# Optimization experiments

Measured on AMD Instinct MI355X. Metric: run time of the kernel, lower is better.

## Reference

```python
import jax, jax.numpy as jnp
import numpy as np

THRESHOLD = 0.01


def setup_inputs() -> dict:
    key = jax.random.key(0)
    kv_cache = jax.random.normal(key, (2, 16, 8192, 128), dtype=jnp.float32)
    return {"kv_cache": kv_cache}


def _dequantize_bin(kv, binmask, levels):
    # min/max restricted to the bin via +-inf sentinels (no dynamic shapes)
    inf = jnp.float32(jnp.inf)
    bmin = jnp.min(jnp.where(binmask, kv, inf))
    bmax = jnp.max(jnp.where(binmask, kv, -inf))
    has_any = jnp.any(binmask)
    valid = has_any & (bmax != bmin)
    denom = jnp.where(valid, bmax - bmin, jnp.float32(1.0))  # safe denom
    q = jnp.round((kv - bmin) / denom * levels)
    deq = q / levels * denom + bmin
    return jnp.where(binmask & valid, deq, kv)


def reference(kv_cache):
    mask = jnp.abs(kv_cache) > THRESHOLD  # large-value bin
    out = _dequantize_bin(kv_cache, ~mask, jnp.float32(15.0))   # small bin: 4-bit
    out = jnp.where(mask, _dequantize_bin(kv_cache, mask, jnp.float32(255.0)), out)  # large bin: 8-bit
    return out
```

## Files before the change

kernel.cpp:

```cpp
#include <hip/hip_runtime.h>

static constexpr float kThresh = 0.01f;
static constexpr int RBLOCKS = 1024;

__device__ __forceinline__ unsigned fkey(float f) {
    unsigned u = __float_as_uint(f);
    return (u & 0x80000000u) ? ~u : (u | 0x80000000u);
}
__device__ __forceinline__ float unkey(unsigned k) {
    unsigned u = (k & 0x80000000u) ? (k & 0x7fffffffu) : ~k;
    return __uint_as_float(u);
}

__device__ __forceinline__ void acc_one(float x, unsigned& smin, unsigned& smax,
                                        unsigned& lmin, unsigned& lmax) {
    unsigned k = fkey(x);
    if (fabsf(x) > kThresh) {
        lmin = min(lmin, k);
        lmax = max(lmax, k);
    } else {
        smin = min(smin, k);
        smax = max(smax, k);
    }
}

__device__ __forceinline__ void wave_reduce4(unsigned& smin, unsigned& smax,
                                             unsigned& lmin, unsigned& lmax) {
    #pragma unroll
    for (int off = 32; off > 0; off >>= 1) {
        smin = min(smin, (unsigned)__shfl_down((int)smin, off));
        smax = max(smax, (unsigned)__shfl_down((int)smax, off));
        lmin = min(lmin, (unsigned)__shfl_down((int)lmin, off));
        lmax = max(lmax, (unsigned)__shfl_down((int)lmax, off));
    }
}

__global__ __launch_bounds__(256) void kv_partial(const float* __restrict__ in, int n,
                                                  unsigned* __restrict__ partials) {
    unsigned smin = 0xFFFFFFFFu, smax = 0u, lmin = 0xFFFFFFFFu, lmax = 0u;
    const int n4 = n >> 2;
    const float4* __restrict__ in4 = (const float4*)in;
    const int stride = gridDim.x * blockDim.x;
    for (int i = blockIdx.x * blockDim.x + threadIdx.x; i < n4; i += stride) {
        float4 v = in4[i];
        acc_one(v.x, smin, smax, lmin, lmax);
        acc_one(v.y, smin, smax, lmin, lmax);
        acc_one(v.z, smin, smax, lmin, lmax);
        acc_one(v.w, smin, smax, lmin, lmax);
    }
    for (int i = (n4 << 2) + blockIdx.x * blockDim.x + threadIdx.x; i < n; i += stride) {
        acc_one(in[i], smin, smax, lmin, lmax);
    }

    wave_reduce4(smin, smax, lmin, lmax);

    __shared__ unsigned ls[4][4];
    const int wave = threadIdx.x >> 6;
    if ((threadIdx.x & 63) == 0) {
        ls[wave][0] = smin; ls[wave][1] = smax; ls[wave][2] = lmin; ls[wave][3] = lmax;
    }
    __syncthreads();
    if (threadIdx.x == 0) {
        unsigned a = ls[0][0], b = ls[0][1], c = ls[0][2], d = ls[0][3];
        #pragma unroll
        for (int w = 1; w < 4; ++w) {
            a = min(a, ls[w][0]); b = max(b, ls[w][1]);
            c = min(c, ls[w][2]); d = max(d, ls[w][3]);
        }
        partials[blockIdx.x * 4 + 0] = a;
        partials[blockIdx.x * 4 + 1] = b;
        partials[blockIdx.x * 4 + 2] = c;
        partials[blockIdx.x * 4 + 3] = d;
    }
}

__global__ __launch_bounds__(256) void kv_final(const unsigned* __restrict__ partials,
                                                unsigned* __restrict__ ws) {
    unsigned smin = 0xFFFFFFFFu, smax = 0u, lmin = 0xFFFFFFFFu, lmax = 0u;
    for (int i = threadIdx.x; i < RBLOCKS; i += 256) {
        smin = min(smin, partials[4 * i + 0]);
        smax = max(smax, partials[4 * i + 1]);
        lmin = min(lmin, partials[4 * i + 2]);
        lmax = max(lmax, partials[4 * i + 3]);
    }
    wave_reduce4(smin, smax, lmin, lmax);

    __shared__ unsigned ls[4][4];
    const int wave = threadIdx.x >> 6;
    if ((threadIdx.x & 63) == 0) {
        ls[wave][0] = smin; ls[wave][1] = smax; ls[wave][2] = lmin; ls[wave][3] = lmax;
    }
    __syncthreads();
    if (threadIdx.x == 0) {
        unsigned a = ls[0][0], b = ls[0][1], c = ls[0][2], d = ls[0][3];
        #pragma unroll
        for (int w = 1; w < 4; ++w) {
            a = min(a, ls[w][0]); b = max(b, ls[w][1]);
            c = min(c, ls[w][2]); d = max(d, ls[w][3]);
        }
        ws[0] = a; ws[1] = b; ws[2] = c; ws[3] = d;
    }
}

__device__ __forceinline__ float deq1(float x, float smin, float ssc, float sis, bool sv,
                                      float lmin, float lsc, float lis, bool lv) {
    bool large = fabsf(x) > kThresh;
    float bmin = large ? lmin : smin;
    float sc   = large ? lsc : ssc;
    float is   = large ? lis : sis;
    bool  v    = large ? lv : sv;
    float q = rintf((x - bmin) * sc);
    float d = fmaf(q, is, bmin);
    return v ? d : x;
}

__global__ __launch_bounds__(256) void kv_dequant(const float* __restrict__ in,
                                                  float* __restrict__ out, int n,
                                                  const unsigned* __restrict__ ws) {
    const unsigned sk0 = ws[0], sk1 = ws[1], lk0 = ws[2], lk1 = ws[3];
    const bool sv = sk0 < sk1;
    const bool lv = lk0 < lk1;
    const float smin = unkey(sk0);
    const float sden = sv ? (unkey(sk1) - smin) : 1.0f;
    const float lmin = unkey(lk0);
    const float lden = lv ? (unkey(lk1) - lmin) : 1.0f;
    const float ssc = 15.0f / sden,  sis = sden / 15.0f;
    const float lsc = 255.0f / lden, lis = lden / 255.0f;

    const int n4 = n >> 2;
    const int i = blockIdx.x * blockDim.x + threadIdx.x;
    const float4* __restrict__ in4 = (const float4*)in;
    float4* __restrict__ out4 = (float4*)out;
    if (i < n4) {
        float4 v = in4[i];
        float4 r;
        r.x = deq1(v.x, smin, ssc, sis, sv, lmin, lsc, lis, lv);
        r.y = deq1(v.y, smin, ssc, sis, sv, lmin, lsc, lis, lv);
        r.z = deq1(v.z, smin, ssc, sis, sv, lmin, lsc, lis, lv);
        r.w = deq1(v.w, smin, ssc, sis, sv, lmin, lsc, lis, lv);
        out4[i] = r;
    }
    const int tail = n - (n4 << 2);
    if (i < tail) {
        int j = (n4 << 2) + i;
        out[j] = deq1(in[j], smin, ssc, sis, sv, lmin, lsc, lis, lv);
    }
}

extern "C" void kernel_launch(void* const* d_in, const int* in_sizes, int n_in,
                              void* d_out, int out_size, void* d_ws, size_t ws_size,
                              hipStream_t stream) {
    const float* in = (const float*)d_in[0];
    float* out = (float*)d_out;
    unsigned* ws = (unsigned*)d_ws;
    const int n = in_sizes[0];

    unsigned* partials = (unsigned*)d_out;

    kv_partial<<<RBLOCKS, 256, 0, stream>>>(in, n, partials);
    kv_final<<<1, 256, 0, stream>>>(partials, ws);

    const int n4 = n >> 2;
    int dblocks = (n4 + 255) / 256;
    if (dblocks < 1) dblocks = 1;
    kv_dequant<<<dblocks, 256, 0, stream>>>(in, out, n, ws);
}
```

Measured before the change: 243.9 us.

## Fuse min/max reduction and dequantize into one cooperative kernel with grid sync

Replaces the three-kernel sequence (partial reduce, final reduce, dequant) with one cooperative kernel. It computes per-block partials, does a grid-wide sync, has every block re-reduce the partials, then dequantizes with a grid-stride loop. The reduce loop is also unrolled by two to keep more loads in flight. This removes two launch gaps and the separate final pass, and the second read of the 64MB input may partly hit cache. It costs a grid barrier and a cooperative launch, and falls back to the old path if the launch fails or the workspace is too small.

```diff
diff --git a/kernel.cpp b/kernel.cpp
--- a/kernel.cpp
+++ b/kernel.cpp
@@ -1,6 +1,10 @@
 #include <hip/hip_runtime.h>
+#include <hip/hip_cooperative_groups.h>
+
+namespace cg = cooperative_groups;
 
 static constexpr float kThresh = 0.01f;
+static constexpr int FBLOCKS = 1024;
 static constexpr int RBLOCKS = 1024;
 
 __device__ __forceinline__ unsigned fkey(float f) {
@@ -24,6 +28,14 @@
     }
 }
 
+__device__ __forceinline__ void acc4(const float4& v, unsigned& smin, unsigned& smax,
+                                     unsigned& lmin, unsigned& lmax) {
+    acc_one(v.x, smin, smax, lmin, lmax);
+    acc_one(v.y, smin, smax, lmin, lmax);
+    acc_one(v.z, smin, smax, lmin, lmax);
+    acc_one(v.w, smin, smax, lmin, lmax);
+}
+
 __device__ __forceinline__ void wave_reduce4(unsigned& smin, unsigned& smax,
                                              unsigned& lmin, unsigned& lmax) {
     #pragma unroll
@@ -32,73 +44,6 @@
         smax = max(smax, (unsigned)__shfl_down((int)smax, off));
         lmin = min(lmin, (unsigned)__shfl_down((int)lmin, off));
         lmax = max(lmax, (unsigned)__shfl_down((int)lmax, off));
-    }
-}
-
-__global__ __launch_bounds__(256) void kv_partial(const float* __restrict__ in, int n,
-                                                  unsigned* __restrict__ partials) {
-    unsigned smin = 0xFFFFFFFFu, smax = 0u, lmin = 0xFFFFFFFFu, lmax = 0u;
-    const int n4 = n >> 2;
-    const float4* __restrict__ in4 = (const float4*)in;
-    const int stride = gridDim.x * blockDim.x;
-    for (int i = blockIdx.x * blockDim.x + threadIdx.x; i < n4; i += stride) {
-        float4 v = in4[i];
-        acc_one(v.x, smin, smax, lmin, lmax);
-        acc_one(v.y, smin, smax, lmin, lmax);
-        acc_one(v.z, smin, smax, lmin, lmax);
-        acc_one(v.w, smin, smax, lmin, lmax);
-    }
-    for (int i = (n4 << 2) + blockIdx.x * blockDim.x + threadIdx.x; i < n; i += stride) {
-        acc_one(in[i], smin, smax, lmin, lmax);
-    }
-
-    wave_reduce4(smin, smax, lmin, lmax);
-
-    __shared__ unsigned ls[4][4];
-    const int wave = threadIdx.x >> 6;
-    if ((threadIdx.x & 63) == 0) {
-        ls[wave][0] = smin; ls[wave][1] = smax; ls[wave][2] = lmin; ls[wave][3] = lmax;
-    }
-    __syncthreads();
-    if (threadIdx.x == 0) {
-        unsigned a = ls[0][0], b = ls[0][1], c = ls[0][2], d = ls[0][3];
-        #pragma unroll
-        for (int w = 1; w < 4; ++w) {
-            a = min(a, ls[w][0]); b = max(b, ls[w][1]);
-            c = min(c, ls[w][2]); d = max(d, ls[w][3]);
-        }
-        partials[blockIdx.x * 4 + 0] = a;
-        partials[blockIdx.x * 4 + 1] = b;
-        partials[blockIdx.x * 4 + 2] = c;
-        partials[blockIdx.x * 4 + 3] = d;
-    }
-}
-
-__global__ __launch_bounds__(256) void kv_final(const unsigned* __restrict__ partials,
-                                                unsigned* __restrict__ ws) {
-    unsigned smin = 0xFFFFFFFFu, smax = 0u, lmin = 0xFFFFFFFFu, lmax = 0u;
-    for (int i = threadIdx.x; i < RBLOCKS; i += 256) {
-        smin = min(smin, partials[4 * i + 0]);
-        smax = max(smax, partials[4 * i + 1]);
-        lmin = min(lmin, partials[4 * i + 2]);
-        lmax = max(lmax, partials[4 * i + 3]);
-    }
-    wave_reduce4(smin, smax, lmin, lmax);
-
-    __shared__ unsigned ls[4][4];
-    const int wave = threadIdx.x >> 6;
-    if ((threadIdx.x & 63) == 0) {
-        ls[wave][0] = smin; ls[wave][1] = smax; ls[wave][2] = lmin; ls[wave][3] = lmax;
-    }
-    __syncthreads();
-    if (threadIdx.x == 0) {
-        unsigned a = ls[0][0], b = ls[0][1], c = ls[0][2], d = ls[0][3];
-        #pragma unroll
-        for (int w = 1; w < 4; ++w) {
-            a = min(a, ls[w][0]); b = max(b, ls[w][1]);
-            c = min(c, ls[w][2]); d = max(d, ls[w][3]);
-        }
-        ws[0] = a; ws[1] = b; ws[2] = c; ws[3] = d;
     }
 }
 
@@ -112,6 +57,162 @@
     float q = rintf((x - bmin) * sc);
     float d = fmaf(q, is, bmin);
     return v ? d : x;
+}
+
+__global__ __launch_bounds__(256) void kv_fused(const float* __restrict__ in,
+                                                float* __restrict__ out, int n,
+                                                unsigned* __restrict__ ws) {
+    unsigned* __restrict__ partials = ws + 4;
+    const int n4 = n >> 2;
+    const float4* __restrict__ in4 = (const float4*)in;
+    const int stride = gridDim.x * blockDim.x;
+    const int i0 = blockIdx.x * blockDim.x + threadIdx.x;
+
+    unsigned smin = 0xFFFFFFFFu, smax = 0u, lmin = 0xFFFFFFFFu, lmax = 0u;
+    for (int i = i0; i < n4; i += 2 * stride) {
+        float4 a = in4[i];
+        int j = i + stride;
+        float4 b = (j < n4) ? in4[j] : a;
+        acc4(a, smin, smax, lmin, lmax);
+        acc4(b, smin, smax, lmin, lmax);
+    }
+    for (int i = (n4 << 2) + i0; i < n; i += stride) {
+        acc_one(in[i], smin, smax, lmin, lmax);
+    }
+
+    wave_reduce4(smin, smax, lmin, lmax);
+
+    __shared__ unsigned ls[4][4];
+    const int wave = threadIdx.x >> 6;
+    if ((threadIdx.x & 63) == 0) {
+        ls[wave][0] = smin; ls[wave][1] = smax; ls[wave][2] = lmin; ls[wave][3] = lmax;
+    }
+    __syncthreads();
+    if (threadIdx.x == 0) {
+        unsigned a = ls[0][0], b = ls[0][1], c = ls[0][2], d = ls[0][3];
+        #pragma unroll
+        for (int w = 1; w < 4; ++w) {
+            a = min(a, ls[w][0]); b = max(b, ls[w][1]);
+            c = min(c, ls[w][2]); d = max(d, ls[w][3]);
+        }
+        partials[blockIdx.x * 4 + 0] = a;
+        partials[blockIdx.x * 4 + 1] = b;
+        partials[blockIdx.x * 4 + 2] = c;
+        partials[blockIdx.x * 4 + 3] = d;
+    }
+
+    cg::this_grid().sync();
+
+    unsigned fa = 0xFFFFFFFFu, fb = 0u, fc = 0xFFFFFFFFu, fd = 0u;
+    for (int i = threadIdx.x; i < (int)gridDim.x; i += blockDim.x) {
+        fa = min(fa, partials[4 * i + 0]);
+        fb = max(fb, partials[4 * i + 1]);
+        fc = min(fc, partials[4 * i + 2]);
+        fd = max(fd, partials[4 * i + 3]);
+    }
+    wave_reduce4(fa, fb, fc, fd);
+    __syncthreads();
+    if ((threadIdx.x & 63) == 0) {
+        ls[wave][0] = fa; ls[wave][1] = fb; ls[wave][2] = fc; ls[wave][3] = fd;
+    }
+    __syncthreads();
+
+    __shared__ float p_smin, p_ssc, p_sis, p_lmin, p_lsc, p_lis;
+    __shared__ int p_sv, p_lv;
+    if (threadIdx.x == 0) {
+        unsigned a = ls[0][0], b = ls[0][1], c = ls[0][2], d = ls[0][3];
+        #pragma unroll
+        for (int w = 1; w < 4; ++w) {
+            a = min(a, ls[w][0]); b = max(b, ls[w][1]);
+            c = min(c, ls[w][2]); d = max(d, ls[w][3]);
+        }
+        bool sv = a < b, lv = c < d;
+        float smn = unkey(a), lmn = unkey(c);
+        float sden = sv ? (unkey(b) - smn) : 1.0f;
+        float lden = lv ? (unkey(d) - lmn) : 1.0f;
+        p_smin = smn; p_ssc = 15.0f / sden;  p_sis = sden / 15.0f;  p_sv = sv;
+        p_lmin = lmn; p_lsc = 255.0f / lden; p_lis = lden / 255.0f; p_lv = lv;
+    }
+    __syncthreads();
+
+    const float smn = p_smin, ssc = p_ssc, sis = p_sis;
+    const float lmn = p_lmin, lsc = p_lsc, lis = p_lis;
+    const bool sv = p_sv != 0, lv = p_lv != 0;
+
+    float4* __restrict__ out4 = (float4*)out;
+    for (int i = i0; i < n4; i += stride) {
+        float4 v = in4[i];
+        float4 r;
+        r.x = deq1(v.x, smn, ssc, sis, sv, lmn, lsc, lis, lv);
+        r.y = deq1(v.y, smn, ssc, sis, sv, lmn, lsc, lis, lv);
+        r.z = deq1(v.z, smn, ssc, sis, sv, lmn, lsc, lis, lv);
+        r.w = deq1(v.w, smn, ssc, sis, sv, lmn, lsc, lis, lv);
+        out4[i] = r;
+    }
+    for (int i = (n4 << 2) + i0; i < n; i += stride) {
+        out[i] = deq1(in[i], smn, ssc, sis, sv, lmn, lsc, lis, lv);
+    }
+}
+
+__global__ __launch_bounds__(256) void kv_partial(const float* __restrict__ in, int n,
+                                                  unsigned* __restrict__ partials) {
+    unsigned smin = 0xFFFFFFFFu, smax = 0u, lmin = 0xFFFFFFFFu, lmax = 0u;
+    const int n4 = n >> 2;
+    const float4* __restrict__ in4 = (const float4*)in;
+    const int stride = gridDim.x * blockDim.x;
+    for (int i = blockIdx.x * blockDim.x + threadIdx.x; i < n4; i += stride) {
+        float4 v = in4[i];
+        acc4(v, smin, smax, lmin, lmax);
+    }
+    for (int i = (n4 << 2) + blockIdx.x * blockDim.x + threadIdx.x; i < n; i += stride) {
+        acc_one(in[i], smin, smax, lmin, lmax);
+    }
+    wave_reduce4(smin, smax, lmin, lmax);
+    __shared__ unsigned ls[4][4];
+    const int wave = threadIdx.x >> 6;
+    if ((threadIdx.x & 63) == 0) {
+        ls[wave][0] = smin; ls[wave][1] = smax; ls[wave][2] = lmin; ls[wave][3] = lmax;
+    }
+    __syncthreads();
+    if (threadIdx.x == 0) {
+        unsigned a = ls[0][0], b = ls[0][1], c = ls[0][2], d = ls[0][3];
+        #pragma unroll
+        for (int w = 1; w < 4; ++w) {
+            a = min(a, ls[w][0]); b = max(b, ls[w][1]);
+            c = min(c, ls[w][2]); d = max(d, ls[w][3]);
+        }
+        partials[blockIdx.x * 4 + 0] = a;
+        partials[blockIdx.x * 4 + 1] = b;
+        partials[blockIdx.x * 4 + 2] = c;
+        partials[blockIdx.x * 4 + 3] = d;
+    }
+}
+
+__global__ __launch_bounds__(256) void kv_final(const unsigned* __restrict__ partials,
+                                                unsigned* __restrict__ ws) {
+    unsigned smin = 0xFFFFFFFFu, smax = 0u, lmin = 0xFFFFFFFFu, lmax = 0u;
+    for (int i = threadIdx.x; i < RBLOCKS; i += 256) {
+        smin = min(smin, partials[4 * i + 0]);
+        smax = max(smax, partials[4 * i + 1]);
+        lmin = min(lmin, partials[4 * i + 2]);
+        lmax = max(lmax, partials[4 * i + 3]);
+    }
+    wave_reduce4(smin, smax, lmin, lmax);
+    __shared__ unsigned ls[4][4];
+    const int wave = threadIdx.x >> 6;
+    if ((threadIdx.x & 63) == 0) {
+        ls[wave][0] = smin; ls[wave][1] = smax; ls[wave][2] = lmin; ls[wave][3] = lmax;
+    }
+    __syncthreads();
+    if (threadIdx.x == 0) {
+        unsigned a = ls[0][0], b = ls[0][1], c = ls[0][2], d = ls[0][3];
+        #pragma unroll
+        for (int w = 1; w < 4; ++w) {
+            a = min(a, ls[w][0]); b = max(b, ls[w][1]);
+            c = min(c, ls[w][2]); d = max(d, ls[w][3]);
+        }
+        ws[0] = a; ws[1] = b; ws[2] = c; ws[3] = d;
+    }
 }
 
 __global__ __launch_bounds__(256) void kv_dequant(const float* __restrict__ in,
@@ -155,13 +256,22 @@
     unsigned* ws = (unsigned*)d_ws;
     const int n = in_sizes[0];
 
-    unsigned* partials = (unsigned*)d_out;
-
-    kv_partial<<<RBLOCKS, 256, 0, stream>>>(in, n, partials);
-    kv_final<<<1, 256, 0, stream>>>(partials, ws);
-
-    const int n4 = n >> 2;
-    int dblocks = (n4 + 255) / 256;
-    if (dblocks < 1) dblocks = 1;
-    kv_dequant<<<dblocks, 256, 0, stream>>>(in, out, n, ws);
-}
+    const size_t ws_needed = sizeof(unsigned) * (4 + 4 * (size_t)FBLOCKS);
+    bool coop_ok = ws_size >= ws_needed;
+    if (coop_ok) {
+        void* args[] = {(void*)&in, (void*)&out, (void*)&n, (void*)&ws};
+        hipError_t err = hipLaunchCooperativeKernel((void*)kv_fused, dim3(FBLOCKS),
+                                                    dim3(256), args, 0, stream);
+        coop_ok = (err == hipSuccess);
+        if (!coop_ok) (void)hipGetLastError();
+    }
+    if (!coop_ok) {
+        unsigned* partials = (unsigned*)out;
+        kv_partial<<<RBLOCKS, 256, 0, stream>>>(in, n, partials);
+        kv_final<<<1, 256, 0, stream>>>(partials, ws);
+        const int n4 = n >> 2;
+        int dblocks = (n4 + 255) / 256;
+        if (dblocks < 1) dblocks = 1;
+        kv_dequant<<<dblocks, 256, 0, stream>>>(in, out, n, ws);
+    }
+}
```

Result: slower. 340.1 us (+39.5%).
